# Optimization experiments

Hardware: AMD Instinct MI355X
Metric: run time of the kernel (lower is better)

The kernel has to match this reference:

```python
import jax, jax.numpy as jnp
import numpy as np

EPS = 1e-6

def _ln(x):
    # LayerNorm, no affine, eps=1e-6 (biased variance, as in torch)
    mu = jnp.mean(x, axis=-1, keepdims=True)
    var = jnp.mean(jnp.square(x - mu), axis=-1, keepdims=True)
    return (x - mu) * jax.lax.rsqrt(var + EPS)

def _modulate(x, shift, scale):
    return x * (1.0 + scale[:, None, :]) + shift[:, None, :]

def setup_inputs() -> dict:
    key = jax.random.key(0)
    ks = jax.random.split(key, 10)
    B, S, D, F = 8, 1024, 1024, 4096
    s = 0.02
    return {
        "x": jax.random.normal(ks[0], (B, S, D), jnp.float32),
        "c": jax.random.normal(ks[1], (B, D), jnp.float32),
        "w_mod": jax.random.normal(ks[2], (D, 6 * D), jnp.float32) * s,
        "b_mod": jnp.zeros((6 * D,), jnp.float32),
        "w_q": jax.random.normal(ks[3], (D, D), jnp.float32) * s,
        "b_q": jnp.zeros((D,), jnp.float32),
        "w_k": jax.random.normal(ks[4], (D, D), jnp.float32) * s,
        "b_k": jnp.zeros((D,), jnp.float32),
        "w_v": jax.random.normal(ks[5], (D, D), jnp.float32) * s,
        "b_v": jnp.zeros((D,), jnp.float32),
        "w_attn": jax.random.normal(ks[6], (D, D), jnp.float32) * s,
        "b_attn": jnp.zeros((D,), jnp.float32),
        "w_fc1": jax.random.normal(ks[7], (D, F), jnp.float32) * s,
        "b_fc1": jnp.zeros((F,), jnp.float32),
        "w_fc2": jax.random.normal(ks[8], (F, D), jnp.float32) * s,
        "b_fc2": jnp.zeros((D,), jnp.float32),
    }

NUM_HEADS = 16

def reference(x, c, w_mod, b_mod, w_q, b_q, w_k, b_k, w_v, b_v,
              w_attn, b_attn, w_fc1, b_fc1, w_fc2, b_fc2):
    B, S, D = x.shape
    H = NUM_HEADS
    Dh = D // H

    cact = jax.nn.silu(c)                              # [B, D]
    cmod = cact @ w_mod + b_mod                        # [B, 6D]
    (shift_msa, scale_msa, gate_msa,
     shift_mlp, scale_mlp, gate_mlp) = jnp.split(cmod, 6, axis=-1)

    x_norm = _ln(x)                                    # [B, S, D]
    x_modulated = _modulate(x_norm, shift_msa, scale_msa)

    q = (x_modulated @ w_q + b_q).reshape(B, S, H, Dh)
    k = (x_modulated @ w_k + b_k).reshape(B, S, H, Dh)
    v = (x_modulated @ w_v + b_v).reshape(B, S, H, Dh)
    q = q / Dh                                          # note: /head_dim, not /sqrt

    w = jnp.einsum('bqhc,bkhc->bhqk', q, k).astype(jnp.float32)  # [B,H,S,S]
    w = jax.nn.softmax(w, axis=-1)
    y = jnp.einsum('bhqk,bkhc->bqhc', w, v).reshape(B, S, D)

    attn_x = y @ w_attn + b_attn
    x1 = x + gate_msa[:, None, :] * attn_x

    x_norm2 = _ln(x1)
    x_modulated2 = _modulate(x_norm2, shift_mlp, scale_mlp)
    h = jax.nn.gelu(x_modulated2 @ w_fc1 + b_fc1, approximate=False)
    mlp_x = h @ w_fc2 + b_fc2
    x_out = x1 + gate_mlp[:, None, :] * mlp_x

    return (x_out, x_norm, x_modulated, shift_msa, scale_msa, cmod, cact)
```

## Files before the change

kernel.cpp:

```cpp
#include <hip/hip_runtime.h>
#include <math.h>

typedef unsigned short u16;
typedef __bf16 bf16;
typedef bf16 bf16x8 __attribute__((ext_vector_type(8)));
typedef float f32x4 __attribute__((ext_vector_type(4)));

__device__ __forceinline__ float b2f(u16 u) {
    union { unsigned int i; float f; } w;
    w.i = ((unsigned int)u) << 16;
    return w.f;
}
__device__ __forceinline__ u16 f2b(float f) {
    union { float f; unsigned int i; } w;
    w.f = f;
    unsigned int x = w.i;
    return (u16)((x + 0x7fffu + ((x >> 16) & 1u)) >> 16);
}
__device__ __forceinline__ void gload16(const void* g, void* l) {
    __builtin_amdgcn_global_load_lds(
        (const __attribute__((address_space(1))) unsigned int*)g,
        (__attribute__((address_space(3))) unsigned int*)l, 16, 0, 0);
}

__global__ __launch_bounds__(256)
void sniff_kernel(const u16* __restrict__ w, int* __restrict__ flag) {
    __shared__ int s;
    if (threadIdx.x == 0) s = 0;
    __syncthreads();
    int big = 0;
    for (int i = threadIdx.x; i < 2048; i += 256) {
        float v = fabsf(b2f(w[2 * i]));
        if (!(v < 1e6f)) big = 1;
    }
    if (big) atomicOr(&s, 1);
    __syncthreads();
    if (threadIdx.x == 0) flag[0] = s;
}

__global__ __launch_bounds__(256)
void transpose_w4_kernel(const void* __restrict__ W0, const void* __restrict__ W1,
                         const void* __restrict__ W2, const void* __restrict__ W3,
                         const int* __restrict__ flag, u16* __restrict__ oQKV,
                         u16* __restrict__ oA) {
    __shared__ float T[32][33];
    const int z = blockIdx.z;
    const void* W = z == 0 ? W0 : (z == 1 ? W1 : (z == 2 ? W2 : W3));
    u16* out = z == 3 ? oA : (oQKV + (size_t)z * 1024 * 1024);
    const float scale = z == 0 ? (1.f / 64.f) : 1.f;
    const int tx = threadIdx.x & 31, ty = threadIdx.x >> 5;
    const int kt = blockIdx.y * 32, nt = blockIdx.x * 32;
    const int isf = flag[0];
#pragma unroll
    for (int r = 0; r < 4; ++r) {
        int k = kt + ty + r * 8;
        float v = isf ? ((const float*)W)[(size_t)k * 1024 + nt + tx]
                      : b2f(((const u16*)W)[(size_t)k * 1024 + nt + tx]);
        T[ty + r * 8][tx] = v;
    }
    __syncthreads();
#pragma unroll
    for (int r = 0; r < 4; ++r) {
        int n = nt + ty + r * 8;
        out[(size_t)n * 1024 + kt + tx] = f2b(T[tx][ty + r * 8] * scale);
    }
}

__global__ __launch_bounds__(256)
void transpose_w_kernel(const void* __restrict__ W, const int* __restrict__ flag,
                        int K, int N, u16* __restrict__ out) {
    __shared__ float T[32][33];
    const int tx = threadIdx.x & 31, ty = threadIdx.x >> 5;
    const int kt = blockIdx.y * 32, nt = blockIdx.x * 32;
    const int isf = flag[0];
#pragma unroll
    for (int r = 0; r < 4; ++r) {
        int k = kt + ty + r * 8;
        float v = isf ? ((const float*)W)[(size_t)k * N + nt + tx]
                      : b2f(((const u16*)W)[(size_t)k * N + nt + tx]);
        T[ty + r * 8][tx] = v;
    }
    __syncthreads();
#pragma unroll
    for (int r = 0; r < 4; ++r) {
        int n = nt + ty + r * 8;
        out[(size_t)n * K + kt + tx] = f2b(T[tx][ty + r * 8]);
    }
}

__global__ __launch_bounds__(256)
void biasqkv_kernel(const void* __restrict__ bq, const void* __restrict__ bk,
                    const void* __restrict__ bv, const int* __restrict__ flag,
                    float* __restrict__ out) {
    int i = blockIdx.x * 256 + threadIdx.x;
    if (i >= 3072) return;
    const int isf = flag[0];
    const void* src = i < 1024 ? bq : (i < 2048 ? bk : bv);
    int j = i & 1023;
    float v = isf ? ((const float*)src)[j] : b2f(((const u16*)src)[j]);
    if (i < 1024) v *= (1.f / 64.f);
    out[i] = v;
}

__global__ __launch_bounds__(256)
void silu_kernel(const void* __restrict__ c, const int* __restrict__ flag,
                 float* __restrict__ cactf, float* __restrict__ out_cact) {
    int i = blockIdx.x * 256 + threadIdx.x;
    if (i < 8 * 1024) {
        float v = flag[0] ? ((const float*)c)[i] : b2f(((const u16*)c)[i]);
        float s = v / (1.f + expf(-v));
        cactf[i] = s;
        out_cact[i] = s;
    }
}

__global__ __launch_bounds__(256)
void cmod1_kernel(const float* __restrict__ cactf, const void* __restrict__ w_mod,
                  const int* __restrict__ flag, float* __restrict__ partial) {
    __shared__ float sca[8][128];
    const int tid = threadIdx.x;
    const int ks = blockIdx.y;
    if (tid < 128) {
#pragma unroll
        for (int b = 0; b < 8; ++b) sca[b][tid] = cactf[b * 1024 + ks * 128 + tid];
    }
    __syncthreads();
    const int j = blockIdx.x * 256 + tid;
    const int isf = flag[0];
    float acc[8] = {};
    if (isf) {
        const float* wf = (const float*)w_mod + (size_t)(ks * 128) * 6144 + j;
        for (int k = 0; k < 128; ++k) {
            float wv = wf[(size_t)k * 6144];
#pragma unroll
            for (int b = 0; b < 8; ++b) acc[b] = fmaf(sca[b][k], wv, acc[b]);
        }
    } else {
        const u16* wb = (const u16*)w_mod + (size_t)(ks * 128) * 6144 + j;
        for (int k = 0; k < 128; ++k) {
            float wv = b2f(wb[(size_t)k * 6144]);
#pragma unroll
            for (int b = 0; b < 8; ++b) acc[b] = fmaf(sca[b][k], wv, acc[b]);
        }
    }
#pragma unroll
    for (int b = 0; b < 8; ++b) partial[(ks * 8 + b) * 6144 + j] = acc[b];
}

__global__ __launch_bounds__(256)
void cmod2_kernel(const float* __restrict__ partial, const void* __restrict__ b_mod,
                  const int* __restrict__ flag, float* __restrict__ cmodf,
                  float* __restrict__ out_cmod, float* __restrict__ out_shift,
                  float* __restrict__ out_scale) {
    const int j = blockIdx.x * 256 + threadIdx.x;
    const int isf = flag[0];
    float bm = isf ? ((const float*)b_mod)[j] : b2f(((const u16*)b_mod)[j]);
#pragma unroll
    for (int b = 0; b < 8; ++b) {
        float acc = bm;
#pragma unroll
        for (int ks = 0; ks < 8; ++ks) acc += partial[(ks * 8 + b) * 6144 + j];
        cmodf[b * 6144 + j] = acc;
        out_cmod[b * 6144 + j] = acc;
        if (j < 1024) out_shift[b * 1024 + j] = acc;
        else if (j < 2048) out_scale[b * 1024 + (j - 1024)] = acc;
    }
}

__global__ __launch_bounds__(256)
void ln_mod_kernel(const void* __restrict__ xin, const int* __restrict__ flag,
                   int dtype, const float* __restrict__ cmodf,
                   int shift_off, int scale_off, float* __restrict__ out_norm,
                   float* __restrict__ out_mod, u16* __restrict__ ws_mod) {
    const int row = blockIdx.x;
    const int tid = threadIdx.x;
    const int bidx = row >> 10;
    const int isf = (dtype == 2) ? flag[0] : dtype;
    const size_t base = (size_t)row * 1024 + tid * 4;
    float v[4];
    if (isf) {
        float4 f = *reinterpret_cast<const float4*>((const float*)xin + base);
        v[0] = f.x; v[1] = f.y; v[2] = f.z; v[3] = f.w;
    } else {
        ushort4 u = *reinterpret_cast<const ushort4*>((const u16*)xin + base);
        v[0] = b2f(u.x); v[1] = b2f(u.y); v[2] = b2f(u.z); v[3] = b2f(u.w);
    }
    float s = v[0] + v[1] + v[2] + v[3];
#pragma unroll
    for (int o = 32; o; o >>= 1) s += __shfl_xor(s, o, 64);
    __shared__ float red1[4], red2[4];
    const int lane = tid & 63, wv = tid >> 6;
    if (lane == 0) red1[wv] = s;
    __syncthreads();
    float mean = (red1[0] + red1[1] + red1[2] + red1[3]) * 0.0009765625f;
    float d0 = v[0] - mean, d1 = v[1] - mean, d2 = v[2] - mean, d3 = v[3] - mean;
    float sq = d0 * d0 + d1 * d1 + d2 * d2 + d3 * d3;
#pragma unroll
    for (int o = 32; o; o >>= 1) sq += __shfl_xor(sq, o, 64);
    if (lane == 0) red2[wv] = sq;
    __syncthreads();
    float var = (red2[0] + red2[1] + red2[2] + red2[3]) * 0.0009765625f;
    float rs = rsqrtf(var + 1e-6f);
    float xn[4] = {d0 * rs, d1 * rs, d2 * rs, d3 * rs};
    const int d = tid * 4;
    const float* cb = cmodf + bidx * 6144;
    float4 fn = {xn[0], xn[1], xn[2], xn[3]};
    float4 fm;
    fm.x = xn[0] * (1.f + cb[scale_off + d + 0]) + cb[shift_off + d + 0];
    fm.y = xn[1] * (1.f + cb[scale_off + d + 1]) + cb[shift_off + d + 1];
    fm.z = xn[2] * (1.f + cb[scale_off + d + 2]) + cb[shift_off + d + 2];
    fm.w = xn[3] * (1.f + cb[scale_off + d + 3]) + cb[shift_off + d + 3];
    if (out_norm) *reinterpret_cast<float4*>(out_norm + base) = fn;
    if (out_mod)  *reinterpret_cast<float4*>(out_mod + base)  = fm;
    if (ws_mod) {
        ushort4 um = {f2b(fm.x), f2b(fm.y), f2b(fm.z), f2b(fm.w)};
        *reinterpret_cast<ushort4*>(ws_mod + base) = um;
    }
}

template <int MODE>
__global__ __launch_bounds__(256, 2)
void gemm_kernel(const u16* __restrict__ A, const u16* __restrict__ BT,
                 const void* __restrict__ bias, const float* __restrict__ bias32,
                 const int* __restrict__ flag, int M, int N, int K,
                 u16* __restrict__ Cb, const void* __restrict__ Xres,
                 const float* __restrict__ cmodf, int gate_off,
                 u16* __restrict__ x1b, float* __restrict__ outf,
                 u16* __restrict__ VTg) {
    __shared__ __align__(16) u16 Al[128 * 32];
    __shared__ __align__(16) u16 Bl[128 * 32];
    const int tid = threadIdx.x, lane = tid & 63, w = tid >> 6;
    const int m0 = blockIdx.y * 128, n0 = blockIdx.x * 128;
    const int wr = (w & 1) * 64, wc = (w >> 1) * 64;
    const int l15 = lane & 15, kq = (lane >> 4) << 3;
    const int srow = lane >> 2, skoff = (lane & 3) * 8;
    f32x4 acc[4][4] = {};
    for (int k0 = 0; k0 < K; k0 += 32) {
        __syncthreads();
#pragma unroll
        for (int c = 0; c < 2; ++c) {
            const int chunk = w * 2 + c;
            const int row = chunk * 16 + srow;
            gload16(A + (size_t)(m0 + row) * K + k0 + skoff, &Al[chunk * 512]);
            gload16(BT + (size_t)(n0 + row) * K + k0 + skoff, &Bl[chunk * 512]);
        }
        __syncthreads();
        bf16x8 afr[4], bfr[4];
#pragma unroll
        for (int i = 0; i < 4; ++i)
            afr[i] = *(const bf16x8*)&Al[(wr + i * 16 + l15) * 32 + kq];
#pragma unroll
        for (int j = 0; j < 4; ++j)
            bfr[j] = *(const bf16x8*)&Bl[(wc + j * 16 + l15) * 32 + kq];
#pragma unroll
        for (int i = 0; i < 4; ++i)
#pragma unroll
            for (int j = 0; j < 4; ++j)
                acc[i][j] = __builtin_amdgcn_mfma_f32_16x16x32_bf16(
                    afr[i], bfr[j], acc[i][j], 0, 0, 0);
    }
    const int isf = flag[0];
    const int rbase = (lane >> 4) << 2;
#pragma unroll
    for (int i = 0; i < 4; ++i) {
#pragma unroll
        for (int j = 0; j < 4; ++j) {
            const int colbase = n0 + wc + j * 16;
            const int col = colbase + l15;
            float bv;
            if (MODE == 0) bv = bias32[col];
            else bv = isf ? ((const float*)bias)[col] : b2f(((const u16*)bias)[col]);
#pragma unroll
            for (int r = 0; r < 4; ++r) {
                const int m = m0 + wr + i * 16 + rbase + r;
                float t = acc[i][j][r] + bv;
                const size_t idx = (size_t)m * N + col;
                if (MODE == 0) {
                    if (colbase >= 2048) {
                        const int hh = (col - 2048) >> 6, dh = (col - 2048) & 63;
                        const int bb = m >> 10, ss = m & 1023;
                        VTg[(((size_t)bb * 16 + hh) * 64 + dh) * 1024 + ss] = f2b(t);
                    } else {
                        Cb[idx] = f2b(t);
                    }
                } else if (MODE == 1) {
                    const int bb = m >> 10;
                    float g = cmodf[bb * 6144 + gate_off + col];
                    float xr = isf ? ((const float*)Xres)[idx]
                                   : b2f(((const u16*)Xres)[idx]);
                    x1b[idx] = f2b(xr + g * t);
                } else if (MODE == 2) {
                    float gl = 0.5f * t * (1.f + erff(t * 0.70710678118654752f));
                    Cb[idx] = f2b(gl);
                } else {
                    const int bb = m >> 10;
                    float g = cmodf[bb * 6144 + gate_off + col];
                    outf[idx] = b2f(x1b[idx]) + g * t;
                }
            }
        }
    }
}

__global__ __launch_bounds__(256)
void attn_kernel(const u16* __restrict__ QKV, const u16* __restrict__ VT,
                 u16* __restrict__ Y) {
    __shared__ __align__(16) u16 qS[64 * 72];
    __shared__ __align__(16) u16 kS[128 * 72];
    __shared__ __align__(16) u16 vS[64 * 132];
    __shared__ __align__(16) u16 pS[64 * 132];
    const int tid = threadIdx.x, lane = tid & 63, w = tid >> 6;
    const int l15 = lane & 15, quad = lane >> 4;
    const int kq = quad * 8, rbase = quad * 4;
    const int qt = blockIdx.x, h = blockIdx.y, b = blockIdx.z;
    const int s0 = qt * 64;
    const size_t rowbase = (size_t)b * 1024;
    const int hq = h * 64, hk = 1024 + h * 64;
    const u16* vtg = VT + ((size_t)b * 16 + h) * 64 * 1024;
#pragma unroll
    for (int it = 0; it < 2; ++it) {
        int idx = it * 256 + tid;
        int r = idx >> 3, ch = idx & 7;
        *(bf16x8*)&qS[r * 72 + ch * 8] =
            *(const bf16x8*)(QKV + (rowbase + s0 + r) * 3072 + hq + ch * 8);
    }
    __syncthreads();
    bf16x8 qa[2];
#pragma unroll
    for (int ks = 0; ks < 2; ++ks)
        qa[ks] = *(const bf16x8*)&qS[(w * 16 + l15) * 72 + ks * 32 + kq];
    f32x4 accO[4] = {};
    float m_i[4], l_i[4];
#pragma unroll
    for (int r = 0; r < 4; ++r) { m_i[r] = -3e38f; l_i[r] = 0.f; }
    for (int kt = 0; kt < 8; ++kt) {
        __syncthreads();
#pragma unroll
        for (int it = 0; it < 4; ++it) {
            int idx = it * 256 + tid;
            int r = idx >> 3, ch = idx & 7;
            *(bf16x8*)&kS[r * 72 + ch * 8] =
                *(const bf16x8*)(QKV + (rowbase + kt * 128 + r) * 3072 + hk + ch * 8);
        }
#pragma unroll
        for (int it = 0; it < 4; ++it) {
            int idx = it * 256 + tid;
            int dh = idx >> 4, kc = idx & 15;
            *(bf16x8*)&vS[dh * 132 + kc * 8] =
                *(const bf16x8*)(vtg + (size_t)dh * 1024 + kt * 128 + kc * 8);
        }
        __syncthreads();
        f32x4 s[8];
#pragma unroll
        for (int nt = 0; nt < 8; ++nt) {
            f32x4 a = {};
#pragma unroll
            for (int ks = 0; ks < 2; ++ks) {
                bf16x8 kb = *(const bf16x8*)&kS[(nt * 16 + l15) * 72 + ks * 32 + kq];
                a = __builtin_amdgcn_mfma_f32_16x16x32_bf16(qa[ks], kb, a, 0, 0, 0);
            }
            s[nt] = a;
        }
        float alpha[4];
#pragma unroll
        for (int r = 0; r < 4; ++r) {
            float mx = fmaxf(fmaxf(fmaxf(s[0][r], s[1][r]), fmaxf(s[2][r], s[3][r])),
                             fmaxf(fmaxf(s[4][r], s[5][r]), fmaxf(s[6][r], s[7][r])));
            mx = fmaxf(mx, __shfl_xor(mx, 1));
            mx = fmaxf(mx, __shfl_xor(mx, 2));
            mx = fmaxf(mx, __shfl_xor(mx, 4));
            mx = fmaxf(mx, __shfl_xor(mx, 8));
            float mn = fmaxf(m_i[r], mx);
            alpha[r] = __expf(m_i[r] - mn);
            m_i[r] = mn;
            float rs = 0.f;
#pragma unroll
            for (int nt = 0; nt < 8; ++nt) {
                float p = __expf(s[nt][r] - mn);
                s[nt][r] = p;
                rs += p;
            }
            rs += __shfl_xor(rs, 1);
            rs += __shfl_xor(rs, 2);
            rs += __shfl_xor(rs, 4);
            rs += __shfl_xor(rs, 8);
            l_i[r] = l_i[r] * alpha[r] + rs;
        }
#pragma unroll
        for (int nt = 0; nt < 8; ++nt)
#pragma unroll
            for (int r = 0; r < 4; ++r)
                pS[(w * 16 + rbase + r) * 132 + nt * 16 + l15] = f2b(s[nt][r]);
        __syncthreads();
#pragma unroll
        for (int dt = 0; dt < 4; ++dt)
#pragma unroll
            for (int r = 0; r < 4; ++r) accO[dt][r] *= alpha[r];
        bf16x8 pa[4];
#pragma unroll
        for (int ks = 0; ks < 4; ++ks)
            pa[ks] = *(const bf16x8*)&pS[(w * 16 + l15) * 132 + ks * 32 + kq];
#pragma unroll
        for (int dt = 0; dt < 4; ++dt) {
#pragma unroll
            for (int ks = 0; ks < 4; ++ks) {
                bf16x8 vb = *(const bf16x8*)&vS[(dt * 16 + l15) * 132 + ks * 32 + kq];
                accO[dt] = __builtin_amdgcn_mfma_f32_16x16x32_bf16(pa[ks], vb, accO[dt], 0, 0, 0);
            }
        }
    }
#pragma unroll
    for (int dt = 0; dt < 4; ++dt)
#pragma unroll
        for (int r = 0; r < 4; ++r) {
            float o = accO[dt][r] / l_i[r];
            Y[(rowbase + s0 + w * 16 + rbase + r) * 1024 + h * 64 + dt * 16 + l15] = f2b(o);
        }
}

extern "C" void kernel_launch(void* const* d_in, const int* in_sizes, int n_in,
                              void* d_out, int out_size, void* d_ws, size_t ws_size,
                              hipStream_t stream) {
    const void* x      = d_in[0];
    const void* c      = d_in[1];
    const void* w_mod  = d_in[2];
    const void* b_mod  = d_in[3];
    const void* w_q    = d_in[4];
    const void* b_q    = d_in[5];
    const void* w_k    = d_in[6];
    const void* b_k    = d_in[7];
    const void* w_v    = d_in[8];
    const void* b_v    = d_in[9];
    const void* w_attn = d_in[10];
    const void* b_attn = d_in[11];
    const void* w_fc1  = d_in[12];
    const void* b_fc1  = d_in[13];
    const void* w_fc2  = d_in[14];
    const void* b_fc2  = d_in[15];

    float* out = (float*)d_out;
    float* out_xout  = out;
    float* out_norm  = out + 8388608;
    float* out_mod   = out + 16777216;
    float* out_shift = out + 25165824;
    float* out_scale = out + 25174016;
    float* out_cmod  = out + 25182208;
    float* out_cact  = out + 25231360;

    char* ws = (char*)d_ws;
    float* cactf   = (float*)(ws + 0);
    float* cmodf   = (float*)(ws + 32768);
    int*   flag    = (int*)(ws + 229376);
    float* bqkv    = (float*)(ws + 230400);
    float* partial = (float*)(ws + 262144);
    u16* wqkvT = (u16*)(ws + 2097152);
    u16* waT   = (u16*)(ws + 8388608);
    u16* wf1T  = (u16*)(ws + 10485760);
    u16* wf2T  = (u16*)(ws + 18874368);
    u16* xmod  = (u16*)(ws + 27262976);
    u16* yw    = xmod;
    u16* qkv   = (u16*)(ws + 44040192);
    u16* xmod2 = qkv;
    u16* vtg   = (u16*)(ws + 94371840);
    u16* hw    = (u16*)(ws + 60817408);
    u16* x1b   = (u16*)(ws + 127926272);

    sniff_kernel<<<1, 256, 0, stream>>>((const u16*)w_q, flag);
    transpose_w4_kernel<<<dim3(32, 32, 4), 256, 0, stream>>>(w_q, w_k, w_v, w_attn,
        flag, wqkvT, waT);
    transpose_w_kernel<<<dim3(128, 32), 256, 0, stream>>>(w_fc1, flag, 1024, 4096, wf1T);
    transpose_w_kernel<<<dim3(32, 128), 256, 0, stream>>>(w_fc2, flag, 4096, 1024, wf2T);
    biasqkv_kernel<<<12, 256, 0, stream>>>(b_q, b_k, b_v, flag, bqkv);

    silu_kernel<<<32, 256, 0, stream>>>(c, flag, cactf, out_cact);
    cmod1_kernel<<<dim3(24, 8), 256, 0, stream>>>(cactf, w_mod, flag, partial);
    cmod2_kernel<<<24, 256, 0, stream>>>(partial, b_mod, flag, cmodf,
                                         out_cmod, out_shift, out_scale);
    ln_mod_kernel<<<8192, 256, 0, stream>>>(x, flag, 2, cmodf, 0, 1024,
                                            out_norm, out_mod, xmod);
    gemm_kernel<0><<<dim3(24, 64), 256, 0, stream>>>(xmod, wqkvT, nullptr, bqkv,
        flag, 8192, 3072, 1024, qkv, nullptr, nullptr, 0, nullptr, nullptr, vtg);
    attn_kernel<<<dim3(16, 16, 8), 256, 0, stream>>>(qkv, vtg, yw);
    gemm_kernel<1><<<dim3(8, 64), 256, 0, stream>>>(yw, waT, b_attn, nullptr,
        flag, 8192, 1024, 1024, nullptr, x, cmodf, 2048, x1b, nullptr, nullptr);
    ln_mod_kernel<<<8192, 256, 0, stream>>>(x1b, flag, 0, cmodf, 3072, 4096,
                                            nullptr, nullptr, xmod2);
    gemm_kernel<2><<<dim3(32, 64), 256, 0, stream>>>(xmod2, wf1T, b_fc1, nullptr,
        flag, 8192, 4096, 1024, hw, nullptr, nullptr, 0, nullptr, nullptr, nullptr);
    gemm_kernel<3><<<dim3(8, 64), 256, 0, stream>>>(hw, wf2T, b_fc2, nullptr,
        flag, 8192, 1024, 4096, nullptr, nullptr, cmodf, 5120, x1b, out_xout, nullptr);

    (void)in_sizes; (void)n_in; (void)out_size; (void)ws_size;
}
```

Baseline: 730.5 us.

## Prefetch next K/V tiles into registers and load Q directly in attention

```diff
diff --git a/kernel.cpp b/kernel.cpp
--- a/kernel.cpp
+++ b/kernel.cpp
@@ -302,10 +302,9 @@
     }
 }
 
-__global__ __launch_bounds__(256)
+__global__ __launch_bounds__(256, 2)
 void attn_kernel(const u16* __restrict__ QKV, const u16* __restrict__ VT,
                  u16* __restrict__ Y) {
-    __shared__ __align__(16) u16 qS[64 * 72];
     __shared__ __align__(16) u16 kS[128 * 72];
     __shared__ __align__(16) u16 vS[64 * 132];
     __shared__ __align__(16) u16 pS[64 * 132];
@@ -317,18 +316,20 @@
     const size_t rowbase = (size_t)b * 1024;
     const int hq = h * 64, hk = 1024 + h * 64;
     const u16* vtg = VT + ((size_t)b * 16 + h) * 64 * 1024;
-#pragma unroll
-    for (int it = 0; it < 2; ++it) {
+    bf16x8 qa[2];
+#pragma unroll
+    for (int ks = 0; ks < 2; ++ks)
+        qa[ks] = *(const bf16x8*)(QKV + (rowbase + s0 + w * 16 + l15) * 3072 +
+                                  hq + ks * 32 + kq);
+    bf16x8 kreg[4], vreg[4];
+#pragma unroll
+    for (int it = 0; it < 4; ++it) {
         int idx = it * 256 + tid;
         int r = idx >> 3, ch = idx & 7;
-        *(bf16x8*)&qS[r * 72 + ch * 8] =
-            *(const bf16x8*)(QKV + (rowbase + s0 + r) * 3072 + hq + ch * 8);
-    }
-    __syncthreads();
-    bf16x8 qa[2];
-#pragma unroll
-    for (int ks = 0; ks < 2; ++ks)
-        qa[ks] = *(const bf16x8*)&qS[(w * 16 + l15) * 72 + ks * 32 + kq];
+        kreg[it] = *(const bf16x8*)(QKV + (rowbase + r) * 3072 + hk + ch * 8);
+        int dh = idx >> 4, kc = idx & 15;
+        vreg[it] = *(const bf16x8*)(vtg + (size_t)dh * 1024 + kc * 8);
+    }
     f32x4 accO[4] = {};
     float m_i[4], l_i[4];
 #pragma unroll
@@ -339,18 +340,25 @@
         for (int it = 0; it < 4; ++it) {
             int idx = it * 256 + tid;
             int r = idx >> 3, ch = idx & 7;
-            *(bf16x8*)&kS[r * 72 + ch * 8] =
-                *(const bf16x8*)(QKV + (rowbase + kt * 128 + r) * 3072 + hk + ch * 8);
-        }
-#pragma unroll
-        for (int it = 0; it < 4; ++it) {
-            int idx = it * 256 + tid;
+            *(bf16x8*)&kS[r * 72 + ch * 8] = kreg[it];
             int dh = idx >> 4, kc = idx & 15;
-            *(bf16x8*)&vS[dh * 132 + kc * 8] =
-                *(const bf16x8*)(vtg + (size_t)dh * 1024 + kt * 128 + kc * 8);
+            *(bf16x8*)&vS[dh * 132 + kc * 8] = vreg[it];
+        }
+        if (kt < 7) {
+#pragma unroll
+            for (int it = 0; it < 4; ++it) {
+                int idx = it * 256 + tid;
+                int r = idx >> 3, ch = idx & 7;
+                kreg[it] = *(const bf16x8*)(QKV + (rowbase + (kt + 1) * 128 + r) * 3072 +
+                                            hk + ch * 8);
+                int dh = idx >> 4, kc = idx & 15;
+                vreg[it] = *(const bf16x8*)(vtg + (size_t)dh * 1024 +
+                                            (kt + 1) * 128 + kc * 8);
+            }
         }
         __syncthreads();
         f32x4 s[8];
+        __builtin_amdgcn_s_setprio(1);
 #pragma unroll
         for (int nt = 0; nt < 8; ++nt) {
             f32x4 a = {};
@@ -361,6 +369,7 @@
             }
             s[nt] = a;
         }
+        __builtin_amdgcn_s_setprio(0);
         float alpha[4];
 #pragma unroll
         for (int r = 0; r < 4; ++r) {
@@ -400,6 +409,7 @@
 #pragma unroll
         for (int ks = 0; ks < 4; ++ks)
             pa[ks] = *(const bf16x8*)&pS[(w * 16 + l15) * 132 + ks * 32 + kq];
+        __builtin_amdgcn_s_setprio(1);
 #pragma unroll
         for (int dt = 0; dt < 4; ++dt) {
 #pragma unroll
@@ -408,6 +418,7 @@
                 accO[dt] = __builtin_amdgcn_mfma_f32_16x16x32_bf16(pa[ks], vb, accO[dt], 0, 0, 0);
             }
         }
+        __builtin_amdgcn_s_setprio(0);
     }
 #pragma unroll
     for (int dt = 0; dt < 4; ++dt)
```

Result: faster. 707.4 us (-3.2%).
